# Performance work log

Measured on AMD Instinct MI355X. Metric: run time of the kernel, lower is better.

Reference implementation:

```python
import jax, jax.numpy as jnp
import numpy as np

CIN = 28
HID1, HID2 = 64, 64
U_IDX, V_IDX = 11, 12
MU_U, SD_U = 0.02, 0.15
MU_V, SD_V = -0.01, 0.12


def setup_inputs() -> dict:
    key = jax.random.key(0)
    ks = jax.random.split(key, 18)
    B, T, H, W = 8, 8, 128, 128
    s = 0.05
    f32 = jnp.float32
    d = {
        "x": jax.random.normal(ks[0], (B, T, CIN, H, W), f32),
        # reduce: Conv2d(Cin, 24, 1)
        "W_red": jax.random.normal(ks[1], (24, CIN), f32) * s,
        "b_red": jnp.zeros((24,), f32),
        # l1: LSTMCell(24, HID1) + Conv2d(HID1, HID1, 1)
        "Wih1": jax.random.normal(ks[2], (4 * HID1, 24), f32) * s,
        "Whh1": jax.random.normal(ks[3], (4 * HID1, HID1), f32) * s,
        "bih1": jnp.zeros((4 * HID1,), f32),
        "bhh1": jnp.zeros((4 * HID1,), f32),
        "Wc1": jax.random.normal(ks[4], (HID1, HID1), f32) * s,
        "bc1": jnp.zeros((HID1,), f32),
        # l2: LSTMCell(HID1, HID2) + Conv2d(HID2, HID2, 1)
        "Wih2": jax.random.normal(ks[5], (4 * HID2, HID1), f32) * s,
        "Whh2": jax.random.normal(ks[6], (4 * HID2, HID2), f32) * s,
        "bih2": jnp.zeros((4 * HID2,), f32),
        "bhh2": jnp.zeros((4 * HID2,), f32),
        "Wc2": jax.random.normal(ks[7], (HID2, HID2), f32) * s,
        "bc2": jnp.zeros((HID2,), f32),
        # head: Conv2d(HID2, 1, 1)
        "W_head": jax.random.normal(ks[8], (1, HID2), f32) * s,
        "b_head": jnp.zeros((1,), f32),
    }
    return d


def _lstm_cell(flat, h, c, Wih, Whh, bih, bhh):
    # PyTorch LSTMCell gate order: i, f, g, o
    g = flat @ Wih.T + bih + h @ Whh.T + bhh
    i, f, gg, o = jnp.split(g, 4, axis=1)
    c = jax.nn.sigmoid(f) * c + jax.nn.sigmoid(i) * jnp.tanh(gg)
    h = jax.nn.sigmoid(o) * jnp.tanh(c)
    return h, c


def _conv1x1(x, W, b):
    # x: [B,C,H,W], W: [O,C]
    return jnp.einsum('bchw,oc->bohw', x, W) + b[None, :, None, None]


def reference(x, W_red, b_red, Wih1, Whh1, bih1, bhh1, Wc1, bc1,
              Wih2, Whh2, bih2, bhh2, Wc2, bc2, W_head, b_head):
    B, T, C, H, W = x.shape
    N = B * H * W
    # de-normalize u/v channels for every timestep (dropout p=0 -> identity)
    x = x.at[:, :, U_IDX].set(x[:, :, U_IDX] * SD_U + MU_U)
    x = x.at[:, :, V_IDX].set(x[:, :, V_IDX] * SD_V + MU_V)

    def step(carry, frame):
        h1, c1, h2, c2 = carry
        inp = _conv1x1(frame, W_red, b_red)                 # [B,24,H,W]
        flat1 = inp.transpose(0, 2, 3, 1).reshape(N, 24)    # pixel-wise rows
        h1, c1 = _lstm_cell(flat1, h1, c1, Wih1, Whh1, bih1, bhh1)
        h1_map = h1.reshape(B, H, W, HID1).transpose(0, 3, 1, 2)
        o1 = _conv1x1(h1_map, Wc1, bc1)                     # [B,HID1,H,W]
        flat2 = o1.transpose(0, 2, 3, 1).reshape(N, HID1)
        h2, c2 = _lstm_cell(flat2, h2, c2, Wih2, Whh2, bih2, bhh2)
        return (h1, c1, h2, c2), None

    z1 = jnp.zeros((N, HID1), x.dtype)
    z2 = jnp.zeros((N, HID2), x.dtype)
    xs = jnp.transpose(x, (1, 0, 2, 3, 4))                  # [T,B,C,H,W]
    (h1, c1, h2, c2), _ = jax.lax.scan(step, (z1, z1, z2, z2), xs)
    # only the last o2 is used by the head
    h2_map = h2.reshape(B, H, W, HID2).transpose(0, 3, 1, 2)
    o2 = _conv1x1(h2_map, Wc2, bc2)                         # [B,HID2,H,W]
    out = _conv1x1(o2, W_head, b_head)                      # [B,1,H,W]
    return out[:, 0]                                        # squeeze(1) -> [B,H,W]
```

## Files before the change

### kernel.cpp

```cpp
#include <hip/hip_runtime.h>

typedef _Float16 f16;
typedef _Float16 f16x8 __attribute__((ext_vector_type(8)));
typedef float f32x4 __attribute__((ext_vector_type(4)));

#define CIN 28
#define TT 8
#define HW 16384

#define S_SIG  (-1.44269504088896341f)
#define S_TANH ( 2.88539008177792681f)

#define WS_WX    0
#define WS_WHH1  16384
#define WS_W21   49152
#define WS_WHH2  81920
#define WS_BX    114688
#define WS_B2    115712
#define WS_WH    116736
#define WS_BH    116992

__device__ __forceinline__ float lstm_act(float gi, float gf, float gg, float go,
                                          float& c) {
  const float Ei = __builtin_amdgcn_exp2f(gi);
  const float Ef = __builtin_amdgcn_exp2f(gf);
  const float Eg = __builtin_amdgcn_exp2f(gg);
  const float Eo = __builtin_amdgcn_exp2f(go);
  const float rig = __builtin_amdgcn_rcpf((1.f + Ei) * (1.f + Eg));
  const float rf  = __builtin_amdgcn_rcpf(1.f + Ef);
  const float cn  = __builtin_fmaf(rf, c, (Eg - 1.f) * rig);
  c = cn;
  const float Ec  = __builtin_amdgcn_exp2f(cn * S_TANH);
  const float roc = __builtin_amdgcn_rcpf((1.f + Eo) * (1.f + Ec));
  return (Ec - 1.f) * roc;
}

__device__ __forceinline__ void mfma_agf(f32x4& c, f16x8 a, f16x8 b) {
  asm("s_nop 1\n\tv_mfma_f32_16x16x32_f16 %0, %1, %2, %0"
      : "+v"(c) : "v"(a), "a"(b));
}
__device__ __forceinline__ void mfma_ag(f32x4& c, f16x8 a, f16x8 b) {
  asm("v_mfma_f32_16x16x32_f16 %0, %1, %2, %0"
      : "+v"(c) : "v"(a), "a"(b));
}
__device__ __forceinline__ float ag_get(float a) {
  float v; asm("v_accvgpr_read_b32 %0, %1" : "=v"(v) : "a"(a)); return v;
}
__device__ __forceinline__ float ag_put(float v) {
  float a; asm("v_accvgpr_write_b32 %0, %1" : "=a"(a) : "v"(v)); return a;
}

__global__ __launch_bounds__(64) void prep_kernel(
    const float* __restrict__ W_red, const float* __restrict__ b_red,
    const float* __restrict__ Wih1, const float* __restrict__ Whh1,
    const float* __restrict__ bih1, const float* __restrict__ bhh1,
    const float* __restrict__ Wc1,  const float* __restrict__ bc1,
    const float* __restrict__ Wih2, const float* __restrict__ Whh2,
    const float* __restrict__ bih2, const float* __restrict__ bhh2,
    const float* __restrict__ Wc2,  const float* __restrict__ bc2,
    const float* __restrict__ W_head, const float* __restrict__ b_head,
    unsigned char* __restrict__ ws)
{
  const int g = blockIdx.x;
  const int k = threadIdx.x;
  f16* WxH   = (f16*)(ws + WS_WX);
  f16* Whh1H = (f16*)(ws + WS_WHH1);
  f16* W21H  = (f16*)(ws + WS_W21);
  f16* Whh2H = (f16*)(ws + WS_WHH2);
  float* BX  = (float*)(ws + WS_BX);
  float* B2  = (float*)(ws + WS_B2);
  float* WHp = (float*)(ws + WS_WH);
  float* BHp = (float*)(ws + WS_BH);

  const float sc = ((g >> 6) == 2) ? S_TANH : S_SIG;

  float wxv = 0.f;
  if (k < CIN) {
    float s = 0.f;
    for (int r = 0; r < 24; ++r) s += Wih1[g*24 + r] * W_red[r*28 + k];
    wxv = s;
  }
  const float wx11 = __shfl(wxv, 11, 64);
  const float wx12 = __shfl(wxv, 12, 64);
  if (k == 11) wxv *= 0.15f;
  if (k == 12) wxv *= 0.12f;
  if (k < 32) WxH[g*32 + k] = (f16)(wxv * sc);

  Whh1H[g*64 + k] = (f16)(Whh1[g*64 + k] * sc);
  Whh2H[g*64 + k] = (f16)(Whh2[g*64 + k] * sc);

  {
    float s = 0.f;
    for (int m = 0; m < 64; ++m) s += Wih2[g*64 + m] * Wc1[m*64 + k];
    W21H[g*64 + k] = (f16)(s * sc);
  }

  if (k == 0) {
    float bx = bih1[g] + bhh1[g];
    for (int r = 0; r < 24; ++r) bx += Wih1[g*24 + r] * b_red[r];
    bx += wx11 * 0.02f + wx12 * (-0.01f);
    BX[g] = bx * sc;
    float b2v = bih2[g] + bhh2[g];
    for (int m = 0; m < 64; ++m) b2v += Wih2[g*64 + m] * bc1[m];
    B2[g] = b2v * sc;
  }
  if (g == 0) {
    float s = 0.f;
    for (int m = 0; m < 64; ++m) s += W_head[m] * Wc2[m*64 + k];
    WHp[k] = s;
    if (k == 0) {
      float s2 = b_head[0];
      for (int m = 0; m < 64; ++m) s2 += W_head[m] * bc2[m];
      BHp[0] = s2;
    }
  }
}

__global__ __launch_bounds__(256)
__attribute__((amdgpu_waves_per_eu(2, 2)))
void convlstm_main(
    const float* __restrict__ x, const unsigned char* __restrict__ ws,
    float* __restrict__ out)
{
  __shared__ __align__(16) f16 xs[2][64 * 40];
  __shared__ __align__(16) f16 h1buf[2][64 * 72];
  __shared__ __align__(16) f16 h2buf[2][64 * 72];

  const int tid  = threadIdx.x;
  const int lane = tid & 63;
  const int wv   = tid >> 6;
  const int cl   = lane & 15;
  const int qd   = lane >> 4;

  const f16* WxG   = (const f16*)(ws + WS_WX);
  const f16* Whh1G = (const f16*)(ws + WS_WHH1);
  const f16* W21G  = (const f16*)(ws + WS_W21);
  const f16* Whh2G = (const f16*)(ws + WS_WHH2);
  const float* BX  = (const float*)(ws + WS_BX);
  const float* B2  = (const float*)(ws + WS_B2);

  f16x8 wxf[4], whh2v[4];
  f16x8 whh1a[4][2], w21a[4][2], whh2a[4];
  float bxr[4], b2r[4];
#pragma unroll
  for (int P = 0; P < 4; ++P) {
    const int gr = 64*P + 16*wv + cl;
    wxf[P] = *(const f16x8*)(WxG + gr*32 + qd*8);
    whh1a[P][0] = *(const f16x8*)(Whh1G + gr*64 + qd*8);
    whh1a[P][1] = *(const f16x8*)(Whh1G + gr*64 + 32 + qd*8);
    w21a[P][0]  = *(const f16x8*)(W21G  + gr*64 + qd*8);
    w21a[P][1]  = *(const f16x8*)(W21G  + gr*64 + 32 + qd*8);
    whh2a[P]    = *(const f16x8*)(Whh2G + gr*64 + qd*8);
    whh2v[P]    = *(const f16x8*)(Whh2G + gr*64 + 32 + qd*8);
    bxr[P] = BX[gr];
    b2r[P] = B2[gr];
  }

  {
    unsigned* z1 = (unsigned*)&h1buf[0][0];
    unsigned* z2 = (unsigned*)&h2buf[0][0];
#pragma unroll
    for (int i = tid; i < 2304; i += 256) { z1[i] = 0u; z2[i] = 0u; }
  }

  const int gpix = blockIdx.x * 64;
  const float* xb = x + (size_t)(gpix >> 14) * (TT * CIN * HW) + (gpix & (HW - 1));

  const int sp = lane;
  const int cb = wv * 8;

  {
    f16x8 v;
#pragma unroll
    for (int j = 0; j < 8; ++j) {
      const int ch = cb + j;
      v[j] = (ch < CIN) ? (f16)xb[ch*HW + sp] : (f16)0.f;
    }
    *(f16x8*)(&xs[0][sp*40 + cb]) = v;
  }
  __syncthreads();

  float c1s[4][4];
  float c2s[4][4];
#pragma unroll
  for (int a = 0; a < 4; ++a)
#pragma unroll
    for (int b = 0; b < 4; ++b) { c1s[a][b] = 0.f; c2s[a][b] = ag_put(0.f); }

#pragma unroll 1
  for (int t = 0; t < TT; ++t) {
    float xr[8];
    if (t + 1 < TT) {
      const float* xt = xb + (size_t)(t + 1) * (CIN * HW);
#pragma unroll
      for (int j = 0; j < 8; ++j) {
        const int ch = cb + j;
        xr[j] = (ch < CIN) ? xt[ch*HW + sp] : 0.f;
      }
    }

    const f16* xsr = xs[t & 1];
    const f16* h1r = h1buf[t & 1];
    const f16* h2r = h2buf[t & 1];
    f16* h1w = h1buf[(t + 1) & 1];
    f16* h2w = h2buf[(t + 1) & 1];

#pragma unroll
    for (int mb = 0; mb < 4; ++mb) {
      const int p = 16*mb + cl;
      const f16x8 ax  = *(const f16x8*)(xsr + p*40 + qd*8);
      const f16x8 ah0 = *(const f16x8*)(h1r + p*72 + qd*8);
      const f16x8 ah1 = *(const f16x8*)(h1r + p*72 + 32 + qd*8);
      f32x4 acc[4];
#pragma unroll
      for (int P = 0; P < 4; ++P) {
        acc[P] = (f32x4){ bxr[P], bxr[P], bxr[P], bxr[P] };
        mfma_agf(acc[P], ah0, whh1a[P][0]);
        mfma_ag (acc[P], ah1, whh1a[P][1]);
        acc[P] = __builtin_amdgcn_mfma_f32_16x16x32_f16(ax, wxf[P], acc[P], 0, 0, 0);
      }
#pragma unroll
      for (int r = 0; r < 4; ++r) {
        const float hn = lstm_act(acc[0][r], acc[1][r], acc[2][r], acc[3][r],
                                  c1s[mb][r]);
        h1w[(16*mb + 4*qd + r)*72 + 16*wv + cl] = (f16)hn;
      }
    }
    __syncthreads();

    if (t + 1 < TT) {
      f16* xsw = xs[(t + 1) & 1];
      f16x8 v;
#pragma unroll
      for (int j = 0; j < 8; ++j) v[j] = (f16)xr[j];
      *(f16x8*)(xsw + sp*40 + cb) = v;
    }

#pragma unroll
    for (int mb = 0; mb < 4; ++mb) {
      const int p = 16*mb + cl;
      const f16x8 an0 = *(const f16x8*)(h1w + p*72 + qd*8);
      const f16x8 an1 = *(const f16x8*)(h1w + p*72 + 32 + qd*8);
      const f16x8 a20 = *(const f16x8*)(h2r + p*72 + qd*8);
      const f16x8 a21 = *(const f16x8*)(h2r + p*72 + 32 + qd*8);
      f32x4 acc[4];
#pragma unroll
      for (int P = 0; P < 4; ++P) {
        acc[P] = (f32x4){ b2r[P], b2r[P], b2r[P], b2r[P] };
        mfma_agf(acc[P], an0, w21a[P][0]);
        mfma_ag (acc[P], an1, w21a[P][1]);
        mfma_ag (acc[P], a20, whh2a[P]);
        acc[P] = __builtin_amdgcn_mfma_f32_16x16x32_f16(a21, whh2v[P], acc[P], 0, 0, 0);
      }
#pragma unroll
      for (int r = 0; r < 4; ++r) {
        float co = ag_get(c2s[mb][r]);
        const float hn = lstm_act(acc[0][r], acc[1][r], acc[2][r], acc[3][r], co);
        c2s[mb][r] = ag_put(co);
        h2w[(16*mb + 4*qd + r)*72 + 16*wv + cl] = (f16)hn;
      }
    }
    __syncthreads();
  }

  if (tid < 64) {
    const float* wh = (const float*)(ws + WS_WH);
    const f16* row = &h2buf[0][tid * 72];
    float s = *((const float*)(ws + WS_BH));
#pragma unroll
    for (int k = 0; k < 64; ++k) s += (float)row[k] * wh[k];
    out[gpix + tid] = s;
  }
}

extern "C" void kernel_launch(void* const* d_in, const int* in_sizes, int n_in,
                              void* d_out, int out_size, void* d_ws, size_t ws_size,
                              hipStream_t stream) {
  const float* x      = (const float*)d_in[0];
  const float* W_red  = (const float*)d_in[1];
  const float* b_red  = (const float*)d_in[2];
  const float* Wih1   = (const float*)d_in[3];
  const float* Whh1   = (const float*)d_in[4];
  const float* bih1   = (const float*)d_in[5];
  const float* bhh1   = (const float*)d_in[6];
  const float* Wc1    = (const float*)d_in[7];
  const float* bc1    = (const float*)d_in[8];
  const float* Wih2   = (const float*)d_in[9];
  const float* Whh2   = (const float*)d_in[10];
  const float* bih2   = (const float*)d_in[11];
  const float* bhh2   = (const float*)d_in[12];
  const float* Wc2    = (const float*)d_in[13];
  const float* bc2    = (const float*)d_in[14];
  const float* W_head = (const float*)d_in[15];
  const float* b_head = (const float*)d_in[16];

  prep_kernel<<<256, 64, 0, stream>>>(W_red, b_red, Wih1, Whh1, bih1, bhh1,
                                      Wc1, bc1, Wih2, Whh2, bih2, bhh2,
                                      Wc2, bc2, W_head, b_head,
                                      (unsigned char*)d_ws);
  convlstm_main<<<2048, 256, 0, stream>>>(x, (const unsigned char*)d_ws,
                                          (float*)d_out);
}
```

Measured before the change: 377.7 us.

## Stream fragment-ordered weights from global per phase to raise occupancy

Weights are now stored by the prep kernel in MFMA-fragment order, so each lane loads one contiguous f16x8 per fragment. The main kernel no longer keeps all weight sets resident in AGPRs. Layer-1 and layer-2 weights are reloaded from global/L2 each phase, with sched barriers keeping the loads in place, and waves_per_eu is raised from 2 to 3 to cut register pressure and gain occupancy. The LSTM activation also merges two reciprocals into one. The cost is repeated weight loads every timestep, whose latency may not be fully hidden.

```diff
diff --git a/kernel.cpp b/kernel.cpp
--- a/kernel.cpp
+++ b/kernel.cpp
@@ -11,14 +11,14 @@
 #define S_SIG  (-1.44269504088896341f)
 #define S_TANH ( 2.88539008177792681f)
 
-#define WS_WX    0
-#define WS_WHH1  16384
-#define WS_W21   49152
-#define WS_WHH2  81920
-#define WS_BX    114688
-#define WS_B2    115712
-#define WS_WH    116736
-#define WS_BH    116992
+#define WS_WXF    0
+#define WS_WHH1F  16384
+#define WS_W21F   49152
+#define WS_WHH2F  81920
+#define WS_BX     114688
+#define WS_B2     115712
+#define WS_WH     116736
+#define WS_BH     116992
 
 __device__ __forceinline__ float lstm_act(float gi, float gf, float gg, float go,
                                           float& c) {
@@ -26,28 +26,14 @@
   const float Ef = __builtin_amdgcn_exp2f(gf);
   const float Eg = __builtin_amdgcn_exp2f(gg);
   const float Eo = __builtin_amdgcn_exp2f(go);
-  const float rig = __builtin_amdgcn_rcpf((1.f + Ei) * (1.f + Eg));
-  const float rf  = __builtin_amdgcn_rcpf(1.f + Ef);
-  const float cn  = __builtin_fmaf(rf, c, (Eg - 1.f) * rig);
+  const float F  = 1.f + Ef;
+  const float AG = (1.f + Ei) * (1.f + Eg);
+  const float r  = __builtin_amdgcn_rcpf(F * AG);
+  const float cn = __builtin_fmaf(c, r * AG, (Eg - 1.f) * (r * F));
   c = cn;
   const float Ec  = __builtin_amdgcn_exp2f(cn * S_TANH);
   const float roc = __builtin_amdgcn_rcpf((1.f + Eo) * (1.f + Ec));
   return (Ec - 1.f) * roc;
-}
-
-__device__ __forceinline__ void mfma_agf(f32x4& c, f16x8 a, f16x8 b) {
-  asm("s_nop 1\n\tv_mfma_f32_16x16x32_f16 %0, %1, %2, %0"
-      : "+v"(c) : "v"(a), "a"(b));
-}
-__device__ __forceinline__ void mfma_ag(f32x4& c, f16x8 a, f16x8 b) {
-  asm("v_mfma_f32_16x16x32_f16 %0, %1, %2, %0"
-      : "+v"(c) : "v"(a), "a"(b));
-}
-__device__ __forceinline__ float ag_get(float a) {
-  float v; asm("v_accvgpr_read_b32 %0, %1" : "=v"(v) : "a"(a)); return v;
-}
-__device__ __forceinline__ float ag_put(float v) {
-  float a; asm("v_accvgpr_write_b32 %0, %1" : "=a"(a) : "v"(v)); return a;
 }
 
 __global__ __launch_bounds__(64) void prep_kernel(
@@ -63,16 +49,20 @@
 {
   const int g = blockIdx.x;
   const int k = threadIdx.x;
-  f16* WxH   = (f16*)(ws + WS_WX);
-  f16* Whh1H = (f16*)(ws + WS_WHH1);
-  f16* W21H  = (f16*)(ws + WS_W21);
-  f16* Whh2H = (f16*)(ws + WS_WHH2);
+  const int P  = g >> 6, wvv = (g >> 4) & 3, cl = g & 15;
+  const int half = k >> 5, qd = (k >> 3) & 3, j = k & 7;
+  const int lane = qd * 16 + cl;
+
+  f16* WXF   = (f16*)(ws + WS_WXF);
+  f16* WHH1F = (f16*)(ws + WS_WHH1F);
+  f16* W21F  = (f16*)(ws + WS_W21F);
+  f16* WHH2F = (f16*)(ws + WS_WHH2F);
   float* BX  = (float*)(ws + WS_BX);
   float* B2  = (float*)(ws + WS_B2);
   float* WHp = (float*)(ws + WS_WH);
   float* BHp = (float*)(ws + WS_BH);
 
-  const float sc = ((g >> 6) == 2) ? S_TANH : S_SIG;
+  const float sc = (P == 2) ? S_TANH : S_SIG;
 
   float wxv = 0.f;
   if (k < CIN) {
@@ -84,15 +74,16 @@
   const float wx12 = __shfl(wxv, 12, 64);
   if (k == 11) wxv *= 0.15f;
   if (k == 12) wxv *= 0.12f;
-  if (k < 32) WxH[g*32 + k] = (f16)(wxv * sc);
-
-  Whh1H[g*64 + k] = (f16)(Whh1[g*64 + k] * sc);
-  Whh2H[g*64 + k] = (f16)(Whh2[g*64 + k] * sc);
-
+  if (k < 32)
+    WXF[((wvv*4 + P)*64 + lane)*8 + j] = (f16)(wxv * sc);
+
+  const int fidx = (((wvv*4 + P)*2 + half)*64 + lane)*8 + j;
+  WHH1F[fidx] = (f16)(Whh1[g*64 + k] * sc);
+  WHH2F[fidx] = (f16)(Whh2[g*64 + k] * sc);
   {
     float s = 0.f;
     for (int m = 0; m < 64; ++m) s += Wih2[g*64 + m] * Wc1[m*64 + k];
-    W21H[g*64 + k] = (f16)(s * sc);
+    W21F[fidx] = (f16)(s * sc);
   }
 
   if (k == 0) {
@@ -117,7 +108,7 @@
 }
 
 __global__ __launch_bounds__(256)
-__attribute__((amdgpu_waves_per_eu(2, 2)))
+__attribute__((amdgpu_waves_per_eu(3)))
 void convlstm_main(
     const float* __restrict__ x, const unsigned char* __restrict__ ws,
     float* __restrict__ out)
@@ -132,28 +123,16 @@
   const int cl   = lane & 15;
   const int qd   = lane >> 4;
 
-  const f16* WxG   = (const f16*)(ws + WS_WX);
-  const f16* Whh1G = (const f16*)(ws + WS_WHH1);
-  const f16* W21G  = (const f16*)(ws + WS_W21);
-  const f16* Whh2G = (const f16*)(ws + WS_WHH2);
-  const float* BX  = (const float*)(ws + WS_BX);
-  const float* B2  = (const float*)(ws + WS_B2);
-
-  f16x8 wxf[4], whh2v[4];
-  f16x8 whh1a[4][2], w21a[4][2], whh2a[4];
+  const int wx_i  = (wv*4)*64 + lane;
+  const int hh_i  = wv*512 + lane;
+
+  const float* BX = (const float*)(ws + WS_BX);
+  const float* B2 = (const float*)(ws + WS_B2);
   float bxr[4], b2r[4];
 #pragma unroll
   for (int P = 0; P < 4; ++P) {
-    const int gr = 64*P + 16*wv + cl;
-    wxf[P] = *(const f16x8*)(WxG + gr*32 + qd*8);
-    whh1a[P][0] = *(const f16x8*)(Whh1G + gr*64 + qd*8);
-    whh1a[P][1] = *(const f16x8*)(Whh1G + gr*64 + 32 + qd*8);
-    w21a[P][0]  = *(const f16x8*)(W21G  + gr*64 + qd*8);
-    w21a[P][1]  = *(const f16x8*)(W21G  + gr*64 + 32 + qd*8);
-    whh2a[P]    = *(const f16x8*)(Whh2G + gr*64 + qd*8);
-    whh2v[P]    = *(const f16x8*)(Whh2G + gr*64 + 32 + qd*8);
-    bxr[P] = BX[gr];
-    b2r[P] = B2[gr];
+    bxr[P] = BX[64*P + 16*wv + cl];
+    b2r[P] = B2[64*P + 16*wv + cl];
   }
 
   {
@@ -180,12 +159,25 @@
   }
   __syncthreads();
 
-  float c1s[4][4];
-  float c2s[4][4];
+  float c1s[4][4], c2s[4][4];
 #pragma unroll
   for (int a = 0; a < 4; ++a)
 #pragma unroll
-    for (int b = 0; b < 4; ++b) { c1s[a][b] = 0.f; c2s[a][b] = ag_put(0.f); }
+    for (int b = 0; b < 4; ++b) { c1s[a][b] = 0.f; c2s[a][b] = 0.f; }
+
+  f16x8 wxf[4], whh1f[4][2];
+  {
+    const unsigned char* wsl = ws;
+    asm volatile("" : "+s"(wsl));
+    const f16x8* wxB = (const f16x8*)(wsl + WS_WXF);
+    const f16x8* h1B = (const f16x8*)(wsl + WS_WHH1F);
+#pragma unroll
+    for (int P = 0; P < 4; ++P) {
+      wxf[P]      = wxB[wx_i + P*64];
+      whh1f[P][0] = h1B[hh_i + P*128];
+      whh1f[P][1] = h1B[hh_i + P*128 + 64];
+    }
+  }
 
 #pragma unroll 1
   for (int t = 0; t < TT; ++t) {
@@ -215,9 +207,9 @@
 #pragma unroll
       for (int P = 0; P < 4; ++P) {
         acc[P] = (f32x4){ bxr[P], bxr[P], bxr[P], bxr[P] };
-        mfma_agf(acc[P], ah0, whh1a[P][0]);
-        mfma_ag (acc[P], ah1, whh1a[P][1]);
-        acc[P] = __builtin_amdgcn_mfma_f32_16x16x32_f16(ax, wxf[P], acc[P], 0, 0, 0);
+        acc[P] = __builtin_amdgcn_mfma_f32_16x16x32_f16(ah0, whh1f[P][0], acc[P], 0, 0, 0);
+        acc[P] = __builtin_amdgcn_mfma_f32_16x16x32_f16(ah1, whh1f[P][1], acc[P], 0, 0, 0);
+        acc[P] = __builtin_amdgcn_mfma_f32_16x16x32_f16(ax,  wxf[P],      acc[P], 0, 0, 0);
       }
 #pragma unroll
       for (int r = 0; r < 4; ++r) {
@@ -226,7 +218,22 @@
         h1w[(16*mb + 4*qd + r)*72 + 16*wv + cl] = (f16)hn;
       }
     }
-    __syncthreads();
+
+    __builtin_amdgcn_sched_barrier(0);
+    f16x8 w21f[4][2], whh2f[4][2];
+    {
+      const unsigned char* wsl = ws;
+      asm volatile("" : "+s"(wsl));
+      const f16x8* w21B = (const f16x8*)(wsl + WS_W21F);
+      const f16x8* w22B = (const f16x8*)(wsl + WS_WHH2F);
+#pragma unroll
+      for (int P = 0; P < 4; ++P) {
+        w21f[P][0]  = w21B[hh_i + P*128];
+        w21f[P][1]  = w21B[hh_i + P*128 + 64];
+        whh2f[P][0] = w22B[hh_i + P*128];
+        whh2f[P][1] = w22B[hh_i + P*128 + 64];
+      }
+    }
 
     if (t + 1 < TT) {
       f16* xsw = xs[(t + 1) & 1];
@@ -235,6 +242,7 @@
       for (int j = 0; j < 8; ++j) v[j] = (f16)xr[j];
       *(f16x8*)(xsw + sp*40 + cb) = v;
     }
+    __syncthreads();
 
 #pragma unroll
     for (int mb = 0; mb < 4; ++mb) {
@@ -247,17 +255,30 @@
 #pragma unroll
       for (int P = 0; P < 4; ++P) {
         acc[P] = (f32x4){ b2r[P], b2r[P], b2r[P], b2r[P] };
-        mfma_agf(acc[P], an0, w21a[P][0]);
-        mfma_ag (acc[P], an1, w21a[P][1]);
-        mfma_ag (acc[P], a20, whh2a[P]);
-        acc[P] = __builtin_amdgcn_mfma_f32_16x16x32_f16(a21, whh2v[P], acc[P], 0, 0, 0);
+        acc[P] = __builtin_amdgcn_mfma_f32_16x16x32_f16(an0, w21f[P][0],  acc[P], 0, 0, 0);
+        acc[P] = __builtin_amdgcn_mfma_f32_16x16x32_f16(an1, w21f[P][1],  acc[P], 0, 0, 0);
+        acc[P] = __builtin_amdgcn_mfma_f32_16x16x32_f16(a20, whh2f[P][0], acc[P], 0, 0, 0);
+        acc[P] = __builtin_amdgcn_mfma_f32_16x16x32_f16(a21, whh2f[P][1], acc[P], 0, 0, 0);
       }
 #pragma unroll
       for (int r = 0; r < 4; ++r) {
-        float co = ag_get(c2s[mb][r]);
-        const float hn = lstm_act(acc[0][r], acc[1][r], acc[2][r], acc[3][r], co);
-        c2s[mb][r] = ag_put(co);
+        const float hn = lstm_act(acc[0][r], acc[1][r], acc[2][r], acc[3][r],
+                                  c2s[mb][r]);
         h2w[(16*mb + 4*qd + r)*72 + 16*wv + cl] = (f16)hn;
+      }
+    }
+
+    __builtin_amdgcn_sched_barrier(0);
+    if (t + 1 < TT) {
+      const unsigned char* wsl = ws;
+      asm volatile("" : "+s"(wsl));
+      const f16x8* wxB = (const f16x8*)(wsl + WS_WXF);
+      const f16x8* h1B = (const f16x8*)(wsl + WS_WHH1F);
+#pragma unroll
+      for (int P = 0; P < 4; ++P) {
+        wxf[P]      = wxB[wx_i + P*64];
+        whh1f[P][0] = h1B[hh_i + P*128];
+        whh1f[P][1] = h1B[hh_i + P*128 + 64];
       }
     }
     __syncthreads();
```

New measurement: 796.6 us. 2.11x slower.
